# Performance work log

Measured on AMD Instinct MI355X. Metric: run time of the kernel, lower is better.

Reference implementation:

```python
import jax, jax.numpy as jnp
import numpy as np

N_NODES = 100000
N_EDGES = 1600000
NUM_GRAPHS = 4096
EPS = 1e-5


def _glorot(key, shape):
    fan_in, fan_out = shape[0], shape[1]
    lim = float(np.sqrt(6.0 / (fan_in + fan_out)))
    return jax.random.uniform(key, shape, jnp.float32, -lim, lim)


def setup_inputs() -> dict:
    key = jax.random.key(0)
    ks = jax.random.split(key, 32)
    inp = {}
    inp['x'] = jax.random.normal(ks[0], (N_NODES, 32), jnp.float32)
    inp['edge_attr'] = jax.random.uniform(ks[1], (N_EDGES, 8), jnp.float32)
    inp['edge_index'] = jax.random.randint(ks[2], (2, N_EDGES), 0, N_NODES, jnp.int32)
    inp['batch'] = jnp.sort(jax.random.randint(ks[3], (N_NODES,), 0, NUM_GRAPHS, jnp.int32))
    inp['num_graphs'] = NUM_GRAPHS
    # node/edge embeddings
    inp['Wn'] = _glorot(ks[4], (32, 64)); inp['bn_'] = jnp.zeros((64,), jnp.float32)
    inp['We'] = _glorot(ks[5], (8, 16)); inp['be_'] = jnp.zeros((16,), jnp.float32)
    # conv1: 2*64+16=144 -> 128 -> 64
    inp['W1a'] = _glorot(ks[6], (144, 128)); inp['b1a'] = jnp.zeros((128,), jnp.float32)
    inp['W1b'] = _glorot(ks[7], (128, 64)); inp['b1b'] = jnp.zeros((64,), jnp.float32)
    # conv2: 2*64+16=144 -> 64 -> 32
    inp['W2a'] = _glorot(ks[8], (144, 64)); inp['b2a'] = jnp.zeros((64,), jnp.float32)
    inp['W2b'] = _glorot(ks[9], (64, 32)); inp['b2b'] = jnp.zeros((32,), jnp.float32)
    # conv3: 2*32+16=80 -> 32 -> 16
    inp['W3a'] = _glorot(ks[10], (80, 32)); inp['b3a'] = jnp.zeros((32,), jnp.float32)
    inp['W3b'] = _glorot(ks[11], (32, 16)); inp['b3b'] = jnp.zeros((16,), jnp.float32)
    # batchnorm affine params
    inp['g1'] = jnp.ones((64,), jnp.float32); inp['beta1'] = jnp.zeros((64,), jnp.float32)
    inp['g2'] = jnp.ones((32,), jnp.float32); inp['beta2'] = jnp.zeros((32,), jnp.float32)
    inp['g3'] = jnp.ones((16,), jnp.float32); inp['beta3'] = jnp.zeros((16,), jnp.float32)
    # final fc 16 -> 12
    inp['Wfc'] = _glorot(ks[12], (16, 12)); inp['bfc'] = jnp.zeros((12,), jnp.float32)
    return inp


def _conv(x, e_emb, src, dst, Wa, ba, Wb, bb, n_nodes):
    # PyG: x_i = x[target]=x[dst], x_j = x[source]=x[src]; message MLP; mean-aggregate at dst
    m = jnp.concatenate([x[dst], x[src], e_emb], axis=1)      # [E, 2*in+edge]
    m = jax.nn.relu(m @ Wa + ba) @ Wb + bb                    # [E, out]
    s = jax.ops.segment_sum(m, dst, num_segments=n_nodes)
    cnt = jax.ops.segment_sum(jnp.ones((m.shape[0], 1), m.dtype), dst, num_segments=n_nodes)
    return s / jnp.maximum(cnt, 1.0)


def _batchnorm(x, g, b):
    mu = jnp.mean(x, axis=0)
    var = jnp.mean(jnp.square(x - mu), axis=0)
    return (x - mu) * jax.lax.rsqrt(var + EPS) * g + b


def reference(x, edge_attr, edge_index, batch, num_graphs,
              Wn, bn_, We, be_, W1a, b1a, W1b, b1b, W2a, b2a, W2b, b2b,
              W3a, b3a, W3b, b3b, g1, beta1, g2, beta2, g3, beta3, Wfc, bfc):
    n_nodes = x.shape[0]
    src, dst = edge_index[0], edge_index[1]
    e_emb = jax.nn.relu(edge_attr @ We + be_)                 # [E, 16]
    h = jax.nn.relu(x @ Wn + bn_)                             # [N, 64]
    h = _conv(h, e_emb, src, dst, W1a, b1a, W1b, b1b, n_nodes)
    h = jax.nn.relu(_batchnorm(h, g1, beta1))
    h = _conv(h, e_emb, src, dst, W2a, b2a, W2b, b2b, n_nodes)
    h = jax.nn.relu(_batchnorm(h, g2, beta2))
    h = _conv(h, e_emb, src, dst, W3a, b3a, W3b, b3b, n_nodes)
    h = jax.nn.relu(_batchnorm(h, g3, beta3))
    # global mean pool per graph
    s = jax.ops.segment_sum(h, batch, num_segments=num_graphs)
    cnt = jax.ops.segment_sum(jnp.ones((n_nodes, 1), h.dtype), batch, num_segments=num_graphs)
    pooled = s / jnp.maximum(cnt, 1.0)                        # [G, 16]
    return jax.nn.sigmoid(pooled @ Wfc + bfc)                 # [G, 12]
```

## Files before the change

kernel.cpp:

```cpp
#include <hip/hip_runtime.h>
#include <hip/hip_bf16.h>
#include <cstdio>


#define N_NODES 100000
#define N_EDGES 1600000
#define NUM_GRAPHS 4096

typedef unsigned short u16;
typedef unsigned int u32;
typedef _Float16 h2 __attribute__((ext_vector_type(2)));

#if defined(__has_builtin)
#if __has_builtin(__builtin_amdgcn_fdot2)
#define DOT2(a, b, c) __builtin_amdgcn_fdot2((a), (b), (c), false)
#endif
#endif
#ifndef DOT2
#define DOT2(a, b, c) ((c) + (float)(a).x * (float)(b).x + (float)(a).y * (float)(b).y)
#endif

__device__ __forceinline__ float b2f(u16 u) { union { u32 i; float f; } c; c.i = ((u32)u) << 16; return c.f; }
__device__ __forceinline__ float b2f_lo(u32 u) { union { u32 i; float f; } c; c.i = u << 16; return c.f; }
__device__ __forceinline__ float b2f_hi(u32 u) { union { u32 i; float f; } c; c.i = u & 0xffff0000u; return c.f; }
__device__ __forceinline__ u16 f2b(float f) {
    __hip_bfloat16 h = __float2bfloat16(f);
    return *reinterpret_cast<u16*>(&h);
}

template <int CPL>
__device__ __forceinline__ void ld_bf16(const u16* base, float out[CPL]) {
    if constexpr (CPL == 1) {
        out[0] = b2f(*base);
    } else {
        u32 v = *(const u32*)base;
        out[0] = b2f_lo(v); out[1] = b2f_hi(v);
    }
}
template <int CPL>
__device__ __forceinline__ void ld_f32(const float* base, float out[CPL]) {
    if constexpr (CPL == 1) {
        out[0] = *base;
    } else {
        float2 v = *(const float2*)base;
        out[0] = v.x; out[1] = v.y;
    }
}

__global__ __launch_bounds__(256) void hist_k(const int* __restrict__ dst, int* __restrict__ hist) {
    int e = blockIdx.x * 256 + threadIdx.x;
    if (e < N_EDGES) atomicAdd(&hist[dst[e]], 1);
}

__global__ __launch_bounds__(256) void scan_part_k(const int* __restrict__ hist,
        int* __restrict__ excl, int* __restrict__ bsum) {
    __shared__ int sm[256];
    int t = threadIdx.x, b = blockIdx.x;
    int base = b * 1024 + t * 4;
    int v0 = (base + 0 < N_NODES) ? hist[base + 0] : 0;
    int v1 = (base + 1 < N_NODES) ? hist[base + 1] : 0;
    int v2 = (base + 2 < N_NODES) ? hist[base + 2] : 0;
    int v3 = (base + 3 < N_NODES) ? hist[base + 3] : 0;
    int tsum = v0 + v1 + v2 + v3;
    sm[t] = tsum;
    __syncthreads();
    for (int o = 1; o < 256; o <<= 1) {
        int x = (t >= o) ? sm[t - o] : 0;
        __syncthreads();
        sm[t] += x;
        __syncthreads();
    }
    int texcl = sm[t] - tsum;
    if (base + 0 < N_NODES) excl[base + 0] = texcl;
    if (base + 1 < N_NODES) excl[base + 1] = texcl + v0;
    if (base + 2 < N_NODES) excl[base + 2] = texcl + v0 + v1;
    if (base + 3 < N_NODES) excl[base + 3] = texcl + v0 + v1 + v2;
    if (t == 255) bsum[b] = sm[255];
}

__global__ __launch_bounds__(256) void scan_top_k(int* __restrict__ bsum, int* __restrict__ boff,
        int nb, int* __restrict__ row_ptr_last) {
    __shared__ int sm[256];
    int t = threadIdx.x;
    int v = (t < nb) ? bsum[t] : 0;
    sm[t] = v;
    __syncthreads();
    for (int o = 1; o < 256; o <<= 1) {
        int x = (t >= o) ? sm[t - o] : 0;
        __syncthreads();
        sm[t] += x;
        __syncthreads();
    }
    if (t < nb) boff[t] = sm[t] - v;
    if (t == 0) *row_ptr_last = sm[255];
}

__global__ __launch_bounds__(256) void scan_add_k(int* __restrict__ excl, const int* __restrict__ boff,
        int* __restrict__ row_ptr, int* __restrict__ cursor) {
    int i = blockIdx.x * 256 + threadIdx.x;
    if (i >= N_NODES) return;
    int s = excl[i] + boff[i >> 10];
    row_ptr[i] = s;
    cursor[i] = s;
}

__global__ __launch_bounds__(256) void scatter_k(const int* __restrict__ src, const int* __restrict__ dst,
        int* __restrict__ cursor, int* __restrict__ sorted_eid, int* __restrict__ srcs) {
    int e = blockIdx.x * 256 + threadIdx.x;
    if (e < N_EDGES) {
        int p = atomicAdd(&cursor[dst[e]], 1);
        sorted_eid[p] = e;
        srcs[p] = src[e];
    }
}

__global__ __launch_bounds__(256) void ubound_k(const int* __restrict__ row_ptr, int* __restrict__ sn) {
    int u = blockIdx.x * 256 + threadIdx.x;
    if (u > 25000) return;
    if (u == 25000) { sn[u] = N_NODES; return; }
    int target = u * 64;
    int lo = 0, hi = N_NODES;
    while (lo < hi) {
        int mid = (lo + hi) >> 1;
        if (row_ptr[mid] >= target) hi = mid; else lo = mid + 1;
    }
    sn[u] = lo;
}

__global__ __launch_bounds__(256) void edge_emb_k(const float* __restrict__ ea,
        const float* __restrict__ We, const float* __restrict__ be,
        const int* __restrict__ sorted_eid, _Float16* __restrict__ e16s) {
    int idx = blockIdx.x * 256 + threadIdx.x;
    if (idx >= N_EDGES * 16) return;
    int p = idx >> 4, k = idx & 15;
    int e = sorted_eid[p];
    float acc = be[k];
#pragma unroll
    for (int j = 0; j < 8; ++j) acc += ea[(size_t)e * 8 + j] * We[j * 16 + k];
    e16s[idx] = (_Float16)fmaxf(acc, 0.f);
}

__global__ __launch_bounds__(256) void node_emb_k(const float* __restrict__ x,
        const float* __restrict__ Wn, const float* __restrict__ bn_, float* __restrict__ h) {
    int idx = blockIdx.x * 256 + threadIdx.x;
    if (idx >= N_NODES * 64) return;
    int v = idx >> 6, c = idx & 63;
    float acc = bn_[c];
    for (int k = 0; k < 32; ++k) acc += x[(size_t)v * 32 + k] * Wn[(size_t)k * 64 + c];
    h[idx] = fmaxf(acc, 0.f);
}

template <int F, int H>
__global__ __launch_bounds__(256) void proj_k(const float* __restrict__ h,
        const float* __restrict__ Wa, const float* __restrict__ ba,
        float* __restrict__ Pd, u16* __restrict__ Ps) {
    constexpr int C2 = 2 * H;
    constexpr int NPB = 256 / C2;
    constexpr int TILE = 16 * NPB;
    __shared__ float hs[TILE][F];
    const int t = threadIdx.x;
    const int grp = t / C2;
    const int c = t % C2;
    const bool is_src = (c >= H);
    const int cc = is_src ? (c - H) : c;
    float w[F];
    const float* wcol = Wa + (size_t)(is_src ? F : 0) * H + cc;
#pragma unroll
    for (int k = 0; k < F; ++k) w[k] = wcol[(size_t)k * H];
    const float bias = is_src ? 0.f : ba[cc];

    for (int v0 = blockIdx.x * TILE; v0 < N_NODES; v0 += gridDim.x * TILE) {
        __syncthreads();
        for (int i = t; i < TILE * F; i += 256) {
            int vv = v0 + i / F;
            hs[i / F][i % F] = (vv < N_NODES) ? h[(size_t)vv * F + (i % F)] : 0.f;
        }
        __syncthreads();
        const int base = grp * 16;
        const int nmax = (N_NODES - v0 - base >= 16) ? 16
                        : (N_NODES - v0 - base > 0 ? N_NODES - v0 - base : 0);
#pragma unroll 2
        for (int n = 0; n < nmax; ++n) {
            const int v = v0 + base + n;
            const float4* hr4 = (const float4*)hs[base + n];
            float a0 = bias, a1 = 0.f, a2 = 0.f, a3 = 0.f;
#pragma unroll
            for (int k4 = 0; k4 < F / 4; ++k4) {
                float4 hv = hr4[k4];
                a0 += hv.x * w[4 * k4 + 0];
                a1 += hv.y * w[4 * k4 + 1];
                a2 += hv.z * w[4 * k4 + 2];
                a3 += hv.w * w[4 * k4 + 3];
            }
            float acc = (a0 + a1) + (a2 + a3);
            if (is_src) Ps[(size_t)v * H + cc] = f2b(acc);
            else        Pd[(size_t)v * H + cc] = acc;
        }
    }
}

template <int H>
__global__ __launch_bounds__(256) void conv_k(
        const int* __restrict__ sn, const int* __restrict__ row_ptr,
        const int* __restrict__ srcs, const _Float16* __restrict__ e16s,
        float* __restrict__ Pd, const u16* __restrict__ Ps,
        const float* __restrict__ Wae) {
    constexpr int SL = (H >= 64) ? 64 : 32;
    constexpr int NPW = 64 / SL;
    constexpr int CPL = H / SL;
    const int wave = threadIdx.x >> 6, lane = threadIdx.x & 63;
    const int sub = lane / SL;
    const int sl = lane % SL;
    const int c0 = sl * CPL;
    h2 w2h[8][CPL];
#pragma unroll
    for (int k2 = 0; k2 < 8; ++k2)
#pragma unroll
        for (int j = 0; j < CPL; ++j) {
            h2 t;
            t.x = (_Float16)Wae[(2 * k2) * H + c0 + j];
            t.y = (_Float16)Wae[(2 * k2 + 1) * H + c0 + j];
            w2h[k2][j] = t;
        }

    const int uid = (blockIdx.x * 4 + wave) * NPW + sub;
    const int vbeg = sn[uid], vend = sn[uid + 1];

    for (int v = vbeg; v < vend; ++v) {
        const int vv = (SL == 64) ? __builtin_amdgcn_readfirstlane(v) : v;
        float pd[CPL], acc[CPL];
        ld_f32<CPL>(&Pd[(size_t)vv * H + c0], pd);
#pragma unroll
        for (int j = 0; j < CPL; ++j) acc[j] = 0.f;
        const int p0 = row_ptr[vv], p1 = row_ptr[vv + 1];
        const int deg = p1 - p0;

        auto edge = [&](uint4 ra, uint4 rb, const float ps[CPL]) {
            union { u32 u; h2 h; } cv;
            h2 ev[8];
            cv.u = ra.x; ev[0] = cv.h; cv.u = ra.y; ev[1] = cv.h;
            cv.u = ra.z; ev[2] = cv.h; cv.u = ra.w; ev[3] = cv.h;
            cv.u = rb.x; ev[4] = cv.h; cv.u = rb.y; ev[5] = cv.h;
            cv.u = rb.z; ev[6] = cv.h; cv.u = rb.w; ev[7] = cv.h;
            float z[CPL];
#pragma unroll
            for (int j = 0; j < CPL; ++j) z[j] = pd[j] + ps[j];
#pragma unroll
            for (int k2 = 0; k2 < 8; ++k2)
#pragma unroll
                for (int j = 0; j < CPL; ++j) z[j] = DOT2(ev[k2], w2h[k2][j], z[j]);
#pragma unroll
            for (int j = 0; j < CPL; ++j) acc[j] += fmaxf(z[j], 0.f);
        };

        int p = p0;
        for (; p + 3 < p1; p += 4) {
            int s0 = srcs[p], s1 = srcs[p + 1], s2 = srcs[p + 2], s3 = srcs[p + 3];
            const uint4* e0 = (const uint4*)(e16s + (size_t)p * 16);
            uint4 a0 = e0[0], a1 = e0[1];
            uint4 b0 = e0[2], b1 = e0[3];
            uint4 g0 = e0[4], g1 = e0[5];
            uint4 d0 = e0[6], d1 = e0[7];
            float ps0[CPL], ps1[CPL], ps2[CPL], ps3[CPL];
            ld_bf16<CPL>(&Ps[(size_t)s0 * H + c0], ps0);
            ld_bf16<CPL>(&Ps[(size_t)s1 * H + c0], ps1);
            ld_bf16<CPL>(&Ps[(size_t)s2 * H + c0], ps2);
            ld_bf16<CPL>(&Ps[(size_t)s3 * H + c0], ps3);
            edge(a0, a1, ps0);
            edge(b0, b1, ps1);
            edge(g0, g1, ps2);
            edge(d0, d1, ps3);
        }
        for (; p < p1; ++p) {
            int s0 = srcs[p];
            const uint4* e0 = (const uint4*)(e16s + (size_t)p * 16);
            uint4 a0 = e0[0], a1 = e0[1];
            float ps0[CPL];
            ld_bf16<CPL>(&Ps[(size_t)s0 * H + c0], ps0);
            edge(a0, a1, ps0);
        }

        const float invd = (deg > 0) ? 1.f / (float)deg : 0.f;
        if constexpr (CPL == 2) {
            float2 o; o.x = acc[0] * invd; o.y = acc[1] * invd;
            *(float2*)&Pd[(size_t)vv * H + c0] = o;
        } else {
            Pd[(size_t)vv * H + c0] = acc[0] * invd;
        }
    }
}

template <int H, int Fo>
__global__ __launch_bounds__(256) void matvec2_k(const float* __restrict__ m,
        const int* __restrict__ row_ptr,
        const float* __restrict__ Wb, const float* __restrict__ bb,
        float* __restrict__ y, float* __restrict__ stats) {
    constexpr int FoC = (Fo < 32) ? Fo : 32;
    constexpr int CG = Fo / FoC;
    constexpr int NPW = 32 / FoC;
    constexpr int NG = 4 / CG;
    constexpr int SLOTS = NG * NPW;
    constexpr int KH = H / 2;
    constexpr int TILE = 4096 / H;
    constexpr int J = TILE / SLOTS;

    __shared__ float hs[TILE * H];
    __shared__ int ptile[TILE + 1];
    __shared__ float sh[2 * Fo];

    const int t = threadIdx.x;
    const int wave = t >> 6, lane = t & 63;
    const int kh = lane >> 5;
    const int r = lane & 31;
    const int c_lo = r % FoC;
    const int s = r / FoC;
    const int cg = wave % CG;
    const int ng = wave / CG;
    const int c = cg * FoC + c_lo;
    const int slot = ng * NPW + s;

    for (int i = t; i < 2 * Fo; i += 256) sh[i] = 0.f;

    float w[KH];
#pragma unroll
    for (int k = 0; k < KH; ++k) w[k] = Wb[(size_t)(kh * KH + k) * Fo + c];
    const float bias = bb[c];
    float s1 = 0.f, s2 = 0.f;

    const float4* msrc = (const float4*)m;
    float4* hs4 = (float4*)hs;

    for (int v0 = blockIdx.x * TILE; v0 < N_NODES; v0 += gridDim.x * TILE) {
        __syncthreads();
#pragma unroll
        for (int q = t; q < 1024; q += 256) {
            int node = (q * 4) / H;
            float4 val;
            if (v0 + node < N_NODES) val = msrc[(size_t)v0 * (H / 4) + q];
            else { val.x = val.y = val.z = val.w = 0.f; }
            hs4[q] = val;
        }
        for (int i = t; i <= TILE; i += 256) {
            int v = v0 + i;
            ptile[i] = row_ptr[v < N_NODES ? v : N_NODES];
        }
        __syncthreads();

        for (int j = 0; j < J; ++j) {
            const int n = slot + j * SLOTS;
            const int v = v0 + n;
            const float4* hr4 = (const float4*)&hs[n * H + kh * KH];
            float a0 = 0.f, a1 = 0.f, a2 = 0.f, a3 = 0.f;
#pragma unroll
            for (int k4 = 0; k4 < KH / 4; ++k4) {
                float4 hv = hr4[k4];
                a0 += hv.x * w[4 * k4 + 0];
                a1 += hv.y * w[4 * k4 + 1];
                a2 += hv.z * w[4 * k4 + 2];
                a3 += hv.w * w[4 * k4 + 3];
            }
            float half = (a0 + a1) + (a2 + a3);
            float total = half + __shfl_xor(half, 32) + bias;
            if (kh == 0 && v < N_NODES) {
                const int deg = ptile[n + 1] - ptile[n];
                float val = (deg > 0) ? total : 0.f;
                y[(size_t)v * Fo + c] = val;
                s1 += val; s2 += val * val;
            }
        }
    }

    __syncthreads();
    if (kh == 0) {
        atomicAdd(&sh[c], s1);
        atomicAdd(&sh[Fo + c], s2);
    }
    __syncthreads();
    if (t < 2 * Fo) atomicAdd(&stats[t], sh[t]);
}

template <int Fo>
__global__ __launch_bounds__(256) void bnrelu_k(float* __restrict__ y,
        const float* __restrict__ stats, const float* __restrict__ g, const float* __restrict__ beta) {
    int idx = blockIdx.x * 256 + threadIdx.x;
    if (idx >= N_NODES * Fo) return;
    int co = idx % Fo;
    const float invN = 1.0f / (float)N_NODES;
    float mu = stats[co] * invN;
    float ex2 = stats[Fo + co] * invN;
    float var = fmaxf(ex2 - mu * mu, 0.f);
    float rs = rsqrtf(var + 1e-5f);
    y[idx] = fmaxf((y[idx] - mu) * rs * g[co] + beta[co], 0.f);
}

__global__ __launch_bounds__(256) void pool_bn_k(const float* __restrict__ y,
        const float* __restrict__ stats, const float* __restrict__ g, const float* __restrict__ beta,
        const int* __restrict__ batch, float* __restrict__ pool, int* __restrict__ gcnt) {
    int idx = blockIdx.x * 256 + threadIdx.x;
    if (idx >= N_NODES * 16) return;
    int v = idx >> 4, c = idx & 15;
    const float invN = 1.0f / (float)N_NODES;
    float mu = stats[c] * invN;
    float ex2 = stats[16 + c] * invN;
    float var = fmaxf(ex2 - mu * mu, 0.f);
    float rs = rsqrtf(var + 1e-5f);
    float val = fmaxf((y[idx] - mu) * rs * g[c] + beta[c], 0.f);
    int b = batch[v];
    atomicAdd(&pool[b * 16 + c], val);
    if (c == 0) atomicAdd(&gcnt[b], 1);
}

__global__ __launch_bounds__(256) void out_k(const float* __restrict__ pool,
        const int* __restrict__ gcnt, const float* __restrict__ Wfc,
        const float* __restrict__ bfc, float* __restrict__ out) {
    int idx = blockIdx.x * 256 + threadIdx.x;
    if (idx >= NUM_GRAPHS * 12) return;
    int g = idx / 12, o = idx % 12;
    int cnt = gcnt[g];
    float inv = 1.0f / (float)(cnt > 0 ? cnt : 1);
    float acc = bfc[o];
#pragma unroll
    for (int k = 0; k < 16; ++k) acc += pool[g * 16 + k] * inv * Wfc[k * 12 + o];
    out[idx] = 1.0f / (1.0f + expf(-acc));
}

extern "C" void kernel_launch(void* const* d_in, const int* in_sizes, int n_in,
                              void* d_out, int out_size, void* d_ws, size_t ws_size,
                              hipStream_t stream) {
    const size_t N = N_NODES, E = N_EDGES, G = NUM_GRAPHS;
    const float* x = (const float*)d_in[0];
    const float* ea = (const float*)d_in[1];
    const int* ei = (const int*)d_in[2];
    const int* srcv = ei;
    const int* dstv = ei + E;
    const int* batch = (const int*)d_in[3];
    const float* Wn = (const float*)d_in[5];  const float* bn_ = (const float*)d_in[6];
    const float* We = (const float*)d_in[7];  const float* be_ = (const float*)d_in[8];
    const float* W1a = (const float*)d_in[9]; const float* b1a = (const float*)d_in[10];
    const float* W1b = (const float*)d_in[11]; const float* b1b = (const float*)d_in[12];
    const float* W2a = (const float*)d_in[13]; const float* b2a = (const float*)d_in[14];
    const float* W2b = (const float*)d_in[15]; const float* b2b = (const float*)d_in[16];
    const float* W3a = (const float*)d_in[17]; const float* b3a = (const float*)d_in[18];
    const float* W3b = (const float*)d_in[19]; const float* b3b = (const float*)d_in[20];
    const float* g1 = (const float*)d_in[21]; const float* be1 = (const float*)d_in[22];
    const float* g2 = (const float*)d_in[23]; const float* be2 = (const float*)d_in[24];
    const float* g3 = (const float*)d_in[25]; const float* be3 = (const float*)d_in[26];
    const float* Wfc = (const float*)d_in[27]; const float* bfc = (const float*)d_in[28];

    char* base = (char*)d_ws;
    size_t off = 0;
    auto take = [&](size_t bytes) { size_t o = off; off += (bytes + 255) & ~(size_t)255; return o; };
    int* hist = (int*)(base + take(N * 4));
    int* cursor = (int*)(base + take(N * 4));
    int* row_ptr = (int*)(base + take((N + 1) * 4));
    int* bsum = (int*)(base + take(256 * 4));
    int* boff = (int*)(base + take(256 * 4));
    int* sn = (int*)(base + take(25001 * 4));
    int* sorted = (int*)(base + take(E * 4));
    int* srcs = (int*)(base + take(E * 4));
    float* hbuf = (float*)(base + take(N * 64 * 4));
    float* Pd = (float*)(base + take(N * 128 * 4));
    u16* Ps = (u16*)(base + take(N * 128 * 2));
    _Float16* e16s = (_Float16*)(base + take(E * 16 * 2));
    float* stats = (float*)(base + take(256 * 4));
    float* pool = (float*)(base + take(G * 16 * 4));
    int* gcnt = (int*)(base + take(G * 4));
    if (off > ws_size) {
        fprintf(stderr, "kernel_launch: ws too small: need %zu have %zu\n", off, ws_size);
        return;
    }

    const int NB = (N_NODES + 1023) / 1024;

    hipMemsetAsync(hist, 0, N * 4, stream);
    hist_k<<<dim3((E + 255) / 256), dim3(256), 0, stream>>>(dstv, hist);
    scan_part_k<<<dim3(NB), dim3(256), 0, stream>>>(hist, cursor, bsum);
    scan_top_k<<<dim3(1), dim3(256), 0, stream>>>(bsum, boff, NB, &row_ptr[N_NODES]);
    scan_add_k<<<dim3((N + 255) / 256), dim3(256), 0, stream>>>(cursor, boff, row_ptr, cursor);
    scatter_k<<<dim3((E + 255) / 256), dim3(256), 0, stream>>>(srcv, dstv, cursor, sorted, srcs);
    ubound_k<<<dim3((25001 + 255) / 256), dim3(256), 0, stream>>>(row_ptr, sn);

    edge_emb_k<<<dim3((E * 16 + 255) / 256), dim3(256), 0, stream>>>(ea, We, be_, sorted, e16s);
    node_emb_k<<<dim3((N * 64 + 255) / 256), dim3(256), 0, stream>>>(x, Wn, bn_, hbuf);

    proj_k<64, 128><<<dim3(6250), dim3(256), 0, stream>>>(hbuf, W1a, b1a, Pd, Ps);
    conv_k<128><<<dim3(6250), dim3(256), 0, stream>>>(sn, row_ptr, srcs, e16s, Pd, Ps, W1a + 128 * 128);
    hipMemsetAsync(stats, 0, 256 * 4, stream);
    matvec2_k<128, 64><<<dim3(1024), dim3(256), 0, stream>>>(Pd, row_ptr, W1b, b1b, hbuf, stats);
    bnrelu_k<64><<<dim3((N * 64 + 255) / 256), dim3(256), 0, stream>>>(hbuf, stats, g1, be1);

    proj_k<64, 64><<<dim3(3125), dim3(256), 0, stream>>>(hbuf, W2a, b2a, Pd, Ps);
    conv_k<64><<<dim3(6250), dim3(256), 0, stream>>>(sn, row_ptr, srcs, e16s, Pd, Ps, W2a + 128 * 64);
    hipMemsetAsync(stats, 0, 256 * 4, stream);
    matvec2_k<64, 32><<<dim3(1024), dim3(256), 0, stream>>>(Pd, row_ptr, W2b, b2b, hbuf, stats);
    bnrelu_k<32><<<dim3((N * 32 + 255) / 256), dim3(256), 0, stream>>>(hbuf, stats, g2, be2);

    proj_k<32, 32><<<dim3(1563), dim3(256), 0, stream>>>(hbuf, W3a, b3a, Pd, Ps);
    conv_k<32><<<dim3(3125), dim3(256), 0, stream>>>(sn, row_ptr, srcs, e16s, Pd, Ps, W3a + 64 * 32);
    hipMemsetAsync(stats, 0, 256 * 4, stream);
    matvec2_k<32, 16><<<dim3(1024), dim3(256), 0, stream>>>(Pd, row_ptr, W3b, b3b, hbuf, stats);

    hipMemsetAsync(pool, 0, G * 16 * 4, stream);
    hipMemsetAsync(gcnt, 0, G * 4, stream);
    pool_bn_k<<<dim3((N * 16 + 255) / 256), dim3(256), 0, stream>>>(hbuf, stats, g3, be3, batch, pool, gcnt);
    out_k<<<dim3((G * 12 + 255) / 256), dim3(256), 0, stream>>>(pool, gcnt, Wfc, bfc, (float*)d_out);
}
```

Measured before the change: 1.033 ms.

## Fuse edge embedding into CSR scatter and fold BN+ReLU into projections

The edge embedding is now computed inside the scatter kernel and written directly to its sorted CSR slot, so the sorted edge-id array and its indirect gather pass are gone. Batchnorm plus ReLU for layers 1 and 2 is applied while loading the tile inside the next projection kernel, which removes two elementwise read-modify-write passes over the node features. Node embedding moves to a tiled kernel that keeps weights in registers and stages x in shared memory. The cost is that scatter writes of e16s become non-coalesced random rows, and the scatter kernel now launches 16 lanes per edge with only one doing the atomic.

```diff
diff --git a/kernel.cpp b/kernel.cpp
--- a/kernel.cpp
+++ b/kernel.cpp
@@ -104,14 +104,30 @@
     cursor[i] = s;
 }
 
-__global__ __launch_bounds__(256) void scatter_k(const int* __restrict__ src, const int* __restrict__ dst,
-        int* __restrict__ cursor, int* __restrict__ sorted_eid, int* __restrict__ srcs) {
-    int e = blockIdx.x * 256 + threadIdx.x;
-    if (e < N_EDGES) {
-        int p = atomicAdd(&cursor[dst[e]], 1);
-        sorted_eid[p] = e;
+__global__ __launch_bounds__(256) void scatter2_k(const int* __restrict__ src, const int* __restrict__ dst,
+        const float* __restrict__ ea, const float* __restrict__ We, const float* __restrict__ be,
+        int* __restrict__ cursor, int* __restrict__ srcs, _Float16* __restrict__ e16s) {
+    int idx = blockIdx.x * 256 + threadIdx.x;
+    int e = idx >> 4, k = idx & 15;
+    int lane = threadIdx.x & 63;
+    int p = 0;
+    if (k == 0) {
+        p = atomicAdd(&cursor[dst[e]], 1);
         srcs[p] = src[e];
     }
+    p = __shfl(p, lane & 48);
+    float4 a0 = *(const float4*)(ea + (size_t)e * 8);
+    float4 a1 = *(const float4*)(ea + (size_t)e * 8 + 4);
+    float acc = be[k];
+    acc += a0.x * We[0 * 16 + k];
+    acc += a0.y * We[1 * 16 + k];
+    acc += a0.z * We[2 * 16 + k];
+    acc += a0.w * We[3 * 16 + k];
+    acc += a1.x * We[4 * 16 + k];
+    acc += a1.y * We[5 * 16 + k];
+    acc += a1.z * We[6 * 16 + k];
+    acc += a1.w * We[7 * 16 + k];
+    e16s[(size_t)p * 16 + k] = (_Float16)fmaxf(acc, 0.f);
 }
 
 __global__ __launch_bounds__(256) void ubound_k(const int* __restrict__ row_ptr, int* __restrict__ sn) {
@@ -127,38 +143,74 @@
     sn[u] = lo;
 }
 
-__global__ __launch_bounds__(256) void edge_emb_k(const float* __restrict__ ea,
-        const float* __restrict__ We, const float* __restrict__ be,
-        const int* __restrict__ sorted_eid, _Float16* __restrict__ e16s) {
-    int idx = blockIdx.x * 256 + threadIdx.x;
-    if (idx >= N_EDGES * 16) return;
-    int p = idx >> 4, k = idx & 15;
-    int e = sorted_eid[p];
-    float acc = be[k];
-#pragma unroll
-    for (int j = 0; j < 8; ++j) acc += ea[(size_t)e * 8 + j] * We[j * 16 + k];
-    e16s[idx] = (_Float16)fmaxf(acc, 0.f);
-}
-
-__global__ __launch_bounds__(256) void node_emb_k(const float* __restrict__ x,
+__global__ __launch_bounds__(256) void node_emb2_k(const float* __restrict__ x,
         const float* __restrict__ Wn, const float* __restrict__ bn_, float* __restrict__ h) {
-    int idx = blockIdx.x * 256 + threadIdx.x;
-    if (idx >= N_NODES * 64) return;
-    int v = idx >> 6, c = idx & 63;
-    float acc = bn_[c];
-    for (int k = 0; k < 32; ++k) acc += x[(size_t)v * 32 + k] * Wn[(size_t)k * 64 + c];
-    h[idx] = fmaxf(acc, 0.f);
-}
-
-template <int F, int H>
+    constexpr int C = 64, F = 32, TILE = 64;
+    __shared__ float xs[TILE * F];
+    const int t = threadIdx.x;
+    const int grp = t / C;
+    const int c = t % C;
+    float w[F];
+#pragma unroll
+    for (int k = 0; k < F; ++k) w[k] = Wn[(size_t)k * 64 + c];
+    const float bias = bn_[c];
+    const float4* xsrc = (const float4*)x;
+    float4* xs4 = (float4*)xs;
+
+    for (int v0 = blockIdx.x * TILE; v0 < N_NODES; v0 += gridDim.x * TILE) {
+        __syncthreads();
+        for (int i = t; i < TILE * F / 4; i += 256) {
+            int vv = v0 + (i * 4) / F;
+            float4 val;
+            if (vv < N_NODES) val = xsrc[(size_t)v0 * (F / 4) + i];
+            else { val.x = val.y = val.z = val.w = 0.f; }
+            xs4[i] = val;
+        }
+        __syncthreads();
+        const int base = grp * 16;
+        const int nmax = (N_NODES - v0 - base >= 16) ? 16
+                        : (N_NODES - v0 - base > 0 ? N_NODES - v0 - base : 0);
+        for (int n = 0; n < nmax; ++n) {
+            const int v = v0 + base + n;
+            const float4* xr4 = (const float4*)&xs[(base + n) * F];
+            float a0 = bias, a1 = 0.f, a2 = 0.f, a3 = 0.f;
+#pragma unroll
+            for (int k4 = 0; k4 < F / 4; ++k4) {
+                float4 hv = xr4[k4];
+                a0 += hv.x * w[4 * k4 + 0];
+                a1 += hv.y * w[4 * k4 + 1];
+                a2 += hv.z * w[4 * k4 + 2];
+                a3 += hv.w * w[4 * k4 + 3];
+            }
+            h[(size_t)v * 64 + c] = fmaxf((a0 + a1) + (a2 + a3), 0.f);
+        }
+    }
+}
+
+template <int F, int H, bool BN>
 __global__ __launch_bounds__(256) void proj_k(const float* __restrict__ h,
         const float* __restrict__ Wa, const float* __restrict__ ba,
+        const float* __restrict__ stats, const float* __restrict__ g, const float* __restrict__ beta,
         float* __restrict__ Pd, u16* __restrict__ Ps) {
     constexpr int C2 = 2 * H;
     constexpr int NPB = 256 / C2;
     constexpr int TILE = 16 * NPB;
     __shared__ float hs[TILE][F];
+    __shared__ float sc[BN ? F : 1];
+    __shared__ float shv[BN ? F : 1];
     const int t = threadIdx.x;
+    if constexpr (BN) {
+        if (t < F) {
+            const float invN = 1.0f / (float)N_NODES;
+            float mu = stats[t] * invN;
+            float ex2 = stats[F + t] * invN;
+            float var = fmaxf(ex2 - mu * mu, 0.f);
+            float rs = rsqrtf(var + 1e-5f);
+            float scale = rs * g[t];
+            sc[t] = scale;
+            shv[t] = beta[t] - mu * scale;
+        }
+    }
     const int grp = t / C2;
     const int c = t % C2;
     const bool is_src = (c >= H);
@@ -173,7 +225,9 @@
         __syncthreads();
         for (int i = t; i < TILE * F; i += 256) {
             int vv = v0 + i / F;
-            hs[i / F][i % F] = (vv < N_NODES) ? h[(size_t)vv * F + (i % F)] : 0.f;
+            float val = (vv < N_NODES) ? h[(size_t)vv * F + (i % F)] : 0.f;
+            if constexpr (BN) val = fmaxf(val * sc[i % F] + shv[i % F], 0.f);
+            hs[i / F][i % F] = val;
         }
         __syncthreads();
         const int base = grp * 16;
@@ -377,20 +431,6 @@
     }
     __syncthreads();
     if (t < 2 * Fo) atomicAdd(&stats[t], sh[t]);
-}
-
-template <int Fo>
-__global__ __launch_bounds__(256) void bnrelu_k(float* __restrict__ y,
-        const float* __restrict__ stats, const float* __restrict__ g, const float* __restrict__ beta) {
-    int idx = blockIdx.x * 256 + threadIdx.x;
-    if (idx >= N_NODES * Fo) return;
-    int co = idx % Fo;
-    const float invN = 1.0f / (float)N_NODES;
-    float mu = stats[co] * invN;
-    float ex2 = stats[Fo + co] * invN;
-    float var = fmaxf(ex2 - mu * mu, 0.f);
-    float rs = rsqrtf(var + 1e-5f);
-    y[idx] = fmaxf((y[idx] - mu) * rs * g[co] + beta[co], 0.f);
 }
 
 __global__ __launch_bounds__(256) void pool_bn_k(const float* __restrict__ y,
@@ -456,7 +496,6 @@
     int* bsum = (int*)(base + take(256 * 4));
     int* boff = (int*)(base + take(256 * 4));
     int* sn = (int*)(base + take(25001 * 4));
-    int* sorted = (int*)(base + take(E * 4));
     int* srcs = (int*)(base + take(E * 4));
     float* hbuf = (float*)(base + take(N * 64 * 4));
     float* Pd = (float*)(base + take(N * 128 * 4));
@@ -477,25 +516,22 @@
     scan_part_k<<<dim3(NB), dim3(256), 0, stream>>>(hist, cursor, bsum);
     scan_top_k<<<dim3(1), dim3(256), 0, stream>>>(bsum, boff, NB, &row_ptr[N_NODES]);
     scan_add_k<<<dim3((N + 255) / 256), dim3(256), 0, stream>>>(cursor, boff, row_ptr, cursor);
-    scatter_k<<<dim3((E + 255) / 256), dim3(256), 0, stream>>>(srcv, dstv, cursor, sorted, srcs);
+    scatter2_k<<<dim3(E * 16 / 256), dim3(256), 0, stream>>>(srcv, dstv, ea, We, be_, cursor, srcs, e16s);
     ubound_k<<<dim3((25001 + 255) / 256), dim3(256), 0, stream>>>(row_ptr, sn);
 
-    edge_emb_k<<<dim3((E * 16 + 255) / 256), dim3(256), 0, stream>>>(ea, We, be_, sorted, e16s);
-    node_emb_k<<<dim3((N * 64 + 255) / 256), dim3(256), 0, stream>>>(x, Wn, bn_, hbuf);
-
-    proj_k<64, 128><<<dim3(6250), dim3(256), 0, stream>>>(hbuf, W1a, b1a, Pd, Ps);
+    node_emb2_k<<<dim3(1563), dim3(256), 0, stream>>>(x, Wn, bn_, hbuf);
+
+    proj_k<64, 128, false><<<dim3(6250), dim3(256), 0, stream>>>(hbuf, W1a, b1a, nullptr, nullptr, nullptr, Pd, Ps);
     conv_k<128><<<dim3(6250), dim3(256), 0, stream>>>(sn, row_ptr, srcs, e16s, Pd, Ps, W1a + 128 * 128);
     hipMemsetAsync(stats, 0, 256 * 4, stream);
     matvec2_k<128, 64><<<dim3(1024), dim3(256), 0, stream>>>(Pd, row_ptr, W1b, b1b, hbuf, stats);
-    bnrelu_k<64><<<dim3((N * 64 + 255) / 256), dim3(256), 0, stream>>>(hbuf, stats, g1, be1);
-
-    proj_k<64, 64><<<dim3(3125), dim3(256), 0, stream>>>(hbuf, W2a, b2a, Pd, Ps);
+
+    proj_k<64, 64, true><<<dim3(3125), dim3(256), 0, stream>>>(hbuf, W2a, b2a, stats, g1, be1, Pd, Ps);
     conv_k<64><<<dim3(6250), dim3(256), 0, stream>>>(sn, row_ptr, srcs, e16s, Pd, Ps, W2a + 128 * 64);
     hipMemsetAsync(stats, 0, 256 * 4, stream);
     matvec2_k<64, 32><<<dim3(1024), dim3(256), 0, stream>>>(Pd, row_ptr, W2b, b2b, hbuf, stats);
-    bnrelu_k<32><<<dim3((N * 32 + 255) / 256), dim3(256), 0, stream>>>(hbuf, stats, g2, be2);
-
-    proj_k<32, 32><<<dim3(1563), dim3(256), 0, stream>>>(hbuf, W3a, b3a, Pd, Ps);
+
+    proj_k<32, 32, true><<<dim3(1563), dim3(256), 0, stream>>>(hbuf, W3a, b3a, stats, g2, be2, Pd, Ps);
     conv_k<32><<<dim3(3125), dim3(256), 0, stream>>>(sn, row_ptr, srcs, e16s, Pd, Ps, W3a + 64 * 32);
     hipMemsetAsync(stats, 0, 256 * 4, stream);
     matvec2_k<32, 16><<<dim3(1024), dim3(256), 0, stream>>>(Pd, row_ptr, W3b, b3b, hbuf, stats);
```

New measurement: 1.003 ms. 1.03x faster.
